# Optimization experiments

Measured on AMD Instinct MI355X. Metric: run time of the kernel, lower is better.

## Reference

```python
import jax, jax.numpy as jnp
import numpy as np


def setup_inputs() -> dict:
    key = jax.random.key(0)
    k1, k2, k3 = jax.random.split(key, 3)
    B, N, D = 4, 4096, 1024
    x = jax.random.normal(k1, (B, N, D), dtype=jnp.float32)
    # torch nn.Linear default init ~ U(-1/sqrt(D), 1/sqrt(D)); scale normals similarly
    scale = 1.0 / np.sqrt(D)
    Wq = jax.random.normal(k2, (D, D), dtype=jnp.float32) * scale
    Wk = jax.random.normal(k3, (D, D), dtype=jnp.float32) * scale
    return {"x": x, "Wq": Wq, "Wk": Wk}


def reference(x, Wq, Wk):
    # torch Linear: y = x @ W.T (weight shape [out, in])
    D = x.shape[-1]
    q = jnp.einsum('bnd,ed->bne', x, Wq)  # [B,N,D]
    k = jnp.einsum('bnd,ed->bne', x, Wk)  # [B,N,D]
    scores = jnp.einsum('bqd,bkd->bqk', q, k) / jnp.sqrt(jnp.float32(D))
    attn = jax.nn.softmax(scores, axis=-1)  # [B,N,N]
    return jnp.einsum('bqk,bkd->bqd', attn, x)
```

## Files before the change

### kernel.cpp

```cpp
#include <hip/hip_runtime.h>
#include <stdint.h>
#include <math.h>

typedef __attribute__((ext_vector_type(8))) short short8;
typedef __attribute__((ext_vector_type(4))) float fx4;
typedef unsigned int u32;

#define MFMA16(a, b, c) __builtin_amdgcn_mfma_f32_16x16x32_bf16(a, b, c, 0, 0, 0)
#define SCL 0.04508422002777948f

#define CFENCE asm volatile("" ::: "memory")

__device__ __forceinline__ unsigned short f2bfu(float f) {
  unsigned u = __builtin_bit_cast(unsigned, f);
  u += 0x7fffu + ((u >> 16) & 1u);
  return (unsigned short)(u >> 16);
}

__device__ __forceinline__ float fast_exp2(float x) {
  float r;
  asm("v_exp_f32 %0, %1" : "=v"(r) : "v"(x));
  return r;
}

__device__ __forceinline__ void gl_lds16(const void* g, void* l) {
  __builtin_amdgcn_global_load_lds(
      (const __attribute__((address_space(1))) u32*)g,
      (__attribute__((address_space(3))) u32*)l, 16, 0, 0);
}

__device__ __forceinline__ void barx() {
  CFENCE;
  __builtin_amdgcn_s_barrier();
  CFENCE;
}

__global__ __launch_bounds__(256) void prep_kernel(const float* __restrict__ x,
                                                   unsigned short* __restrict__ xT,
                                                   unsigned short* __restrict__ xbf) {
  __shared__ float tile[64 * 65];
  const int b = blockIdx.z, n0 = blockIdx.x * 64, d0 = blockIdx.y * 64;
  const int tid = threadIdx.x;
  const float* xb = x + ((size_t)b * 4096 + n0) * 1024 + d0;
#pragma unroll
  for (int i = 0; i < 4; i++) {
    int idx = tid + 256 * i;
    int r = idx >> 4, c4 = (idx & 15) * 4;
    const float4 v = *(const float4*)(xb + (size_t)r * 1024 + c4);
    float* tp = &tile[r * 65 + c4];
    tp[0] = v.x; tp[1] = v.y; tp[2] = v.z; tp[3] = v.w;
    uint2 pkt;
    pkt.x = (u32)f2bfu(v.x) | ((u32)f2bfu(v.y) << 16);
    pkt.y = (u32)f2bfu(v.z) | ((u32)f2bfu(v.w) << 16);
    *(uint2*)(xbf + ((size_t)b * 4096 + n0 + r) * 1024 + d0 + c4) = pkt;
  }
  __syncthreads();
  unsigned short* xo = xT + ((size_t)b * 1024 + d0) * 4096 + n0;
#pragma unroll
  for (int i = 0; i < 4; i++) {
    int idx = tid + 256 * i;
    int dr = idx >> 4, n4 = (idx & 15) * 4;
    unsigned short h0 = f2bfu(tile[(n4 + 0) * 65 + dr]);
    unsigned short h1 = f2bfu(tile[(n4 + 1) * 65 + dr]);
    unsigned short h2 = f2bfu(tile[(n4 + 2) * 65 + dr]);
    unsigned short h3 = f2bfu(tile[(n4 + 3) * 65 + dr]);
    uint2 pkt;
    pkt.x = (u32)h0 | ((u32)h1 << 16);
    pkt.y = (u32)h2 | ((u32)h3 << 16);
    *(uint2*)(xo + (size_t)dr * 4096 + n4) = pkt;
  }
}

__global__ __launch_bounds__(256) void wconv_kernel(const float* __restrict__ Wq,
                                                    const float* __restrict__ Wk,
                                                    unsigned short* __restrict__ Wqb,
                                                    unsigned short* __restrict__ Wkb) {
  int gid = blockIdx.x * 256 + threadIdx.x;
  const float* s = (gid < 262144) ? Wq : Wk;
  unsigned short* d = (gid < 262144) ? Wqb : Wkb;
  int off = (gid & 262143) * 4;
  const float4 v = *(const float4*)(s + off);
  uint2 pkt;
  pkt.x = (u32)f2bfu(v.x) | ((u32)f2bfu(v.y) << 16);
  pkt.y = (u32)f2bfu(v.z) | ((u32)f2bfu(v.w) << 16);
  *(uint2*)(d + off) = pkt;
}

__device__ __forceinline__ void core256(const unsigned short* __restrict__ Ab,
                                        const unsigned short* __restrict__ Bb,
                                        char* lp, fx4 (&acc)[8][4]) {
  constexpr int NT = 16;
  const int tid = threadIdx.x;
  const int wave = tid >> 6, lane = tid & 63;
  const int wm = wave >> 2, wn = wave & 3;
  const int quad = lane >> 4, l16 = lane & 15;

  const int sr0 = tid >> 3, so0 = (tid & 7) ^ (sr0 & 7);
  const int ga0 = sr0 * 1024 + so0 * 8;
  const int ga1 = ga0 + 64 * 1024;
  const int ld0 = tid * 16;

  const int cst0 = (quad ^ (l16 & 7)) * 16;
  const int cst1 = ((4 + quad) ^ (l16 & 7)) * 16;
  const int arb = wm * 16384 + l16 * 128;
  const int brb = 32768 + (wn >> 1) * 16384 + (wn & 1) * 8192 + l16 * 128;

#pragma unroll
  for (int i = 0; i < 8; i++)
#pragma unroll
    for (int j = 0; j < 4; j++) acc[i][j] = (fx4)0.f;

#define C_STG(OPb, halfb, rowadd, bufb, kte)                                        \
  do {                                                                              \
    gl_lds16(OPb + (size_t)(rowadd) * 1024 + (kte) + ga0, lp + (bufb) + (halfb) + ld0); \
    gl_lds16(OPb + (size_t)(rowadd) * 1024 + (kte) + ga1,                           \
             lp + (bufb) + (halfb) + ld0 + 8192);                                   \
  } while (0)

  C_STG(Bb, 32768, 0, 0, 0);
  C_STG(Ab, 0, 0, 0, 0);
  C_STG(Ab, 16384, 128, 0, 0);
  C_STG(Bb, 49152, 128, 0, 0);
  C_STG(Bb, 32768, 0, 65536, 64);
  C_STG(Ab, 0, 0, 65536, 64);
  asm volatile("s_waitcnt vmcnt(4)" ::: "memory");
  barx();

  short8 af[8], bf0[4], bf1[4];
  for (int t = 0; t < NT; ++t) {
    const int cbo = (t & 1) * 65536, nbo = cbo ^ 65536;
    const int kt1 = ((t + 1) & (NT - 1)) * 64;
    const int kt2 = ((t + 2) & (NT - 1)) * 64;
#pragma unroll
    for (int mt = 0; mt < 4; mt++) {
      af[2 * mt] = *(const short8*)(lp + cbo + arb + mt * 2048 + cst0);
      af[2 * mt + 1] = *(const short8*)(lp + cbo + arb + mt * 2048 + cst1);
    }
#pragma unroll
    for (int nt = 0; nt < 2; nt++) {
      bf0[2 * nt] = *(const short8*)(lp + cbo + brb + nt * 2048 + cst0);
      bf0[2 * nt + 1] = *(const short8*)(lp + cbo + brb + nt * 2048 + cst1);
    }
    C_STG(Ab, 16384, 128, nbo, kt1);
    barx();
    __builtin_amdgcn_s_setprio(1);
#pragma unroll
    for (int mt = 0; mt < 4; mt++)
#pragma unroll
      for (int nt = 0; nt < 2; nt++) {
        acc[mt][nt] = MFMA16(af[2 * mt], bf0[2 * nt], acc[mt][nt]);
        acc[mt][nt] = MFMA16(af[2 * mt + 1], bf0[2 * nt + 1], acc[mt][nt]);
      }
    __builtin_amdgcn_s_setprio(0);
    barx();
#pragma unroll
    for (int nt = 0; nt < 2; nt++) {
      bf1[2 * nt] = *(const short8*)(lp + cbo + brb + (nt + 2) * 2048 + cst0);
      bf1[2 * nt + 1] = *(const short8*)(lp + cbo + brb + (nt + 2) * 2048 + cst1);
    }
    C_STG(Bb, 49152, 128, nbo, kt1);
    barx();
    __builtin_amdgcn_s_setprio(1);
#pragma unroll
    for (int mt = 0; mt < 4; mt++)
#pragma unroll
      for (int nt = 0; nt < 2; nt++) {
        acc[mt][nt + 2] = MFMA16(af[2 * mt], bf1[2 * nt], acc[mt][nt + 2]);
        acc[mt][nt + 2] = MFMA16(af[2 * mt + 1], bf1[2 * nt + 1], acc[mt][nt + 2]);
      }
    __builtin_amdgcn_s_setprio(0);
    barx();
#pragma unroll
    for (int mt = 0; mt < 4; mt++) {
      af[2 * mt] = *(const short8*)(lp + cbo + arb + (mt + 4) * 2048 + cst0);
      af[2 * mt + 1] = *(const short8*)(lp + cbo + arb + (mt + 4) * 2048 + cst1);
    }
    C_STG(Bb, 32768, 0, cbo, kt2);
    barx();
    __builtin_amdgcn_s_setprio(1);
#pragma unroll
    for (int mt = 0; mt < 4; mt++)
#pragma unroll
      for (int nt = 0; nt < 2; nt++) {
        acc[mt + 4][nt + 2] = MFMA16(af[2 * mt], bf1[2 * nt], acc[mt + 4][nt + 2]);
        acc[mt + 4][nt + 2] = MFMA16(af[2 * mt + 1], bf1[2 * nt + 1], acc[mt + 4][nt + 2]);
      }
    __builtin_amdgcn_s_setprio(0);
    barx();
    C_STG(Ab, 0, 0, cbo, kt2);
    asm volatile("s_waitcnt vmcnt(4)" ::: "memory");
    barx();
    __builtin_amdgcn_s_setprio(1);
#pragma unroll
    for (int mt = 0; mt < 4; mt++)
#pragma unroll
      for (int nt = 0; nt < 2; nt++) {
        acc[mt + 4][nt] = MFMA16(af[2 * mt], bf0[2 * nt], acc[mt + 4][nt]);
        acc[mt + 4][nt] = MFMA16(af[2 * mt + 1], bf0[2 * nt + 1], acc[mt + 4][nt]);
      }
    __builtin_amdgcn_s_setprio(0);
    barx();
  }
#undef C_STG
}

template <int ONES, int NT, int LDA, int LDB>
__device__ __forceinline__ void core128(const unsigned short* __restrict__ Ab,
                                        const unsigned short* __restrict__ Bb,
                                        short* lds, fx4 (&acc)[4][4], fx4 (&accl)[4]) {
  constexpr int BUFB = 49152;
  const int tid = threadIdx.x;
  const int wave = tid >> 6, lane = tid & 63;
  const int wm = wave >> 1, wn = wave & 1;
  const int quad = lane >> 4, l16 = lane & 15;
  char* lp = (char*)lds;

  const int sr0 = tid >> 3, so0 = (tid & 7) ^ (sr0 & 7);
  const int ga0 = sr0 * LDA + so0 * 8;
  const int ga1 = ga0 + 64 * LDA;
  const int gb0 = sr0 * LDB + so0 * 8;
  const int ld0 = tid * 16;

  const int cst0 = (quad ^ (l16 & 7)) * 16;
  const int cst1 = ((4 + quad) ^ (l16 & 7)) * 16;
  const int arb = (wm >> 1) * 16384 + (wm & 1) * 8192 + l16 * 128;
  const int brb = 32768 + wn * 8192 + l16 * 128;

  short8 ones;
#pragma unroll
  for (int i = 0; i < 8; i++) ones[i] = (short)0x3F80;
#pragma unroll
  for (int i = 0; i < 4; i++) {
    accl[i] = (fx4)0.f;
#pragma unroll
    for (int j = 0; j < 4; j++) acc[i][j] = (fx4)0.f;
  }

#define PV_STGA(halfb, rowadd, bufb, kte)                                          \
  do {                                                                             \
    gl_lds16(Ab + (size_t)(rowadd) * LDA + (kte) + ga0, lp + (bufb) + (halfb) + ld0); \
    gl_lds16(Ab + (size_t)(rowadd) * LDA + (kte) + ga1,                            \
             lp + (bufb) + (halfb) + ld0 + 8192);                                  \
  } while (0)
#define PV_STGB(halfb, rowadd, bufb, kte) \
  gl_lds16(Bb + (size_t)(rowadd) * LDB + (kte) + gb0, lp + (bufb) + 32768 + (halfb) + ld0)

  PV_STGB(0, 0, 0, 0);
  PV_STGA(0, 0, 0, 0);
  PV_STGA(16384, 128, 0, 0);
  PV_STGB(8192, 64, 0, 0);
  PV_STGB(0, 0, BUFB, 64);
  PV_STGA(0, 0, BUFB, 64);
  asm volatile("s_waitcnt vmcnt(3)" ::: "memory");
  barx();

  short8 af[4], bf0[4], bf1[4];
  for (int t = 0; t < NT; ++t) {
    const int cbo = (t & 1) * BUFB, nbo = cbo ^ BUFB;
    const int kt1 = ((t + 1) & (NT - 1)) * 64;
    const int kt2 = ((t + 2) & (NT - 1)) * 64;
#pragma unroll
    for (int mt = 0; mt < 2; mt++) {
      af[2 * mt] = *(const short8*)(lp + cbo + arb + mt * 2048 + cst0);
      af[2 * mt + 1] = *(const short8*)(lp + cbo + arb + mt * 2048 + cst1);
    }
#pragma unroll
    for (int nt = 0; nt < 2; nt++) {
      bf0[2 * nt] = *(const short8*)(lp + cbo + brb + nt * 2048 + cst0);
      bf0[2 * nt + 1] = *(const short8*)(lp + cbo + brb + nt * 2048 + cst1);
    }
    PV_STGA(16384, 128, nbo, kt1);
    barx();
    __builtin_amdgcn_s_setprio(1);
#pragma unroll
    for (int mt = 0; mt < 2; mt++) {
#pragma unroll
      for (int nt = 0; nt < 2; nt++) {
        acc[mt][nt] = MFMA16(af[2 * mt], bf0[2 * nt], acc[mt][nt]);
        acc[mt][nt] = MFMA16(af[2 * mt + 1], bf0[2 * nt + 1], acc[mt][nt]);
      }
      if (ONES) {
        accl[mt] = MFMA16(af[2 * mt], ones, accl[mt]);
        accl[mt] = MFMA16(af[2 * mt + 1], ones, accl[mt]);
      }
    }
    __builtin_amdgcn_s_setprio(0);
    barx();
#pragma unroll
    for (int nt = 0; nt < 2; nt++) {
      bf1[2 * nt] = *(const short8*)(lp + cbo + brb + (nt + 2) * 2048 + cst0);
      bf1[2 * nt + 1] = *(const short8*)(lp + cbo + brb + (nt + 2) * 2048 + cst1);
    }
    PV_STGB(8192, 64, nbo, kt1);
    barx();
    __builtin_amdgcn_s_setprio(1);
#pragma unroll
    for (int mt = 0; mt < 2; mt++)
#pragma unroll
      for (int nt = 0; nt < 2; nt++) {
        acc[mt][nt + 2] = MFMA16(af[2 * mt], bf1[2 * nt], acc[mt][nt + 2]);
        acc[mt][nt + 2] = MFMA16(af[2 * mt + 1], bf1[2 * nt + 1], acc[mt][nt + 2]);
      }
    __builtin_amdgcn_s_setprio(0);
    barx();
#pragma unroll
    for (int mt = 0; mt < 2; mt++) {
      af[2 * mt] = *(const short8*)(lp + cbo + arb + (mt + 2) * 2048 + cst0);
      af[2 * mt + 1] = *(const short8*)(lp + cbo + arb + (mt + 2) * 2048 + cst1);
    }
    PV_STGB(0, 0, cbo, kt2);
    barx();
    __builtin_amdgcn_s_setprio(1);
#pragma unroll
    for (int mt = 0; mt < 2; mt++) {
#pragma unroll
      for (int nt = 0; nt < 2; nt++) {
        acc[mt + 2][nt + 2] = MFMA16(af[2 * mt], bf1[2 * nt], acc[mt + 2][nt + 2]);
        acc[mt + 2][nt + 2] = MFMA16(af[2 * mt + 1], bf1[2 * nt + 1], acc[mt + 2][nt + 2]);
      }
      if (ONES) {
        accl[mt + 2] = MFMA16(af[2 * mt], ones, accl[mt + 2]);
        accl[mt + 2] = MFMA16(af[2 * mt + 1], ones, accl[mt + 2]);
      }
    }
    __builtin_amdgcn_s_setprio(0);
    barx();
    PV_STGA(0, 0, cbo, kt2);
    asm volatile("s_waitcnt vmcnt(3)" ::: "memory");
    barx();
    __builtin_amdgcn_s_setprio(1);
#pragma unroll
    for (int mt = 0; mt < 2; mt++)
#pragma unroll
      for (int nt = 0; nt < 2; nt++) {
        acc[mt + 2][nt] = MFMA16(af[2 * mt], bf0[2 * nt], acc[mt + 2][nt]);
        acc[mt + 2][nt] = MFMA16(af[2 * mt + 1], bf0[2 * nt + 1], acc[mt + 2][nt]);
      }
    __builtin_amdgcn_s_setprio(0);
    barx();
  }
#undef PV_STGA
#undef PV_STGB
}

__global__ __launch_bounds__(512) void proj_kernel(
    const unsigned short* __restrict__ xbf, const unsigned short* __restrict__ Wqb,
    const unsigned short* __restrict__ Wkb, unsigned short* __restrict__ Qo,
    unsigned short* __restrict__ Ko) {
  __shared__ __attribute__((aligned(16))) short lds[65536];
  const unsigned short* Wb = blockIdx.z ? Wkb : Wqb;
  unsigned short* O = blockIdx.z ? Ko : Qo;
  const int m0 = blockIdx.x * 256, e0 = blockIdx.y * 256;
  fx4 acc[8][4];
  core256(xbf + (size_t)m0 * 1024, Wb + (size_t)e0 * 1024, (char*)lds, acc);
  const int wave = threadIdx.x >> 6, lane = threadIdx.x & 63;
  const int wm = wave >> 2, wn = wave & 3;
  const int quad = lane >> 4, l16 = lane & 15;
#pragma unroll
  for (int mt = 0; mt < 8; mt++) {
    const int row = m0 + wm * 128 + mt * 16 + quad * 4;
#pragma unroll
    for (int nt = 0; nt < 4; nt++) {
      const int col = e0 + wn * 64 + nt * 16 + l16;
      unsigned short* op = O + (size_t)row * 1024 + col;
#pragma unroll
      for (int i = 0; i < 4; i++) op[(size_t)i * 1024] = f2bfu(acc[mt][nt][i]);
    }
  }
}

__global__ __launch_bounds__(512) void qk_kernel(
    const unsigned short* __restrict__ Qb, const unsigned short* __restrict__ Kb,
    unsigned short* __restrict__ Pp, int bbase) {
  __shared__ __attribute__((aligned(16))) short lds[65536];
  const int bz = blockIdx.z, b = bbase + bz;
  unsigned short* Pb = Pp + (size_t)bz * 4096 * 4096;
  const int m0 = blockIdx.x * 256, n0 = blockIdx.y * 256;
  fx4 acc[8][4];
  core256(Qb + (size_t)b * 4096 * 1024 + (size_t)m0 * 1024,
          Kb + (size_t)b * 4096 * 1024 + (size_t)n0 * 1024, (char*)lds, acc);
  const int wave = threadIdx.x >> 6, lane = threadIdx.x & 63;
  const int wm = wave >> 2, wn = wave & 3;
  const int quad = lane >> 4, l16 = lane & 15;
#pragma unroll
  for (int mt = 0; mt < 8; mt++) {
    const int row = m0 + wm * 128 + mt * 16 + quad * 4;
#pragma unroll
    for (int nt = 0; nt < 4; nt++) {
      const int col = n0 + wn * 64 + nt * 16 + l16;
      unsigned short* pp = Pb + (size_t)row * 4096 + col;
#pragma unroll
      for (int i = 0; i < 4; i++)
        pp[(size_t)i * 4096] = f2bfu(fast_exp2(acc[mt][nt][i] * SCL));
    }
  }
}

__global__ __launch_bounds__(512) void pv_kernel(
    const unsigned short* __restrict__ P, const unsigned short* __restrict__ xT,
    unsigned short* __restrict__ Ost, int bbase) {
  __shared__ __attribute__((aligned(16))) short lds[49152];
  const int bz = blockIdx.z, b = bbase + bz;
  const int m0 = blockIdx.x * 256, e0 = blockIdx.y * 128;
  const unsigned short* Ab = P + (size_t)bz * 4096 * 4096 + (size_t)m0 * 4096;
  const unsigned short* Bb = xT + (size_t)b * 1024 * 4096 + (size_t)e0 * 4096;
  fx4 acc[4][4], accl[4];
  core128<1, 64, 4096, 4096>(Ab, Bb, lds, acc, accl);
  unsigned short* O = Ost + (size_t)b * 4096 * 1024;
  const int wave = threadIdx.x >> 6, lane = threadIdx.x & 63;
  const int wm = wave >> 1, wn = wave & 1;
  const int quad = lane >> 4, l16 = lane & 15;
#pragma unroll
  for (int mt = 0; mt < 4; mt++) {
    const int row = m0 + wm * 64 + mt * 16 + quad * 4;
    const fx4 li = accl[mt];
    fx4 r;
#pragma unroll
    for (int i = 0; i < 4; i++) r[i] = __builtin_amdgcn_rcpf(li[i]);
#pragma unroll
    for (int nt = 0; nt < 4; nt++) {
      const int col = e0 + wn * 64 + nt * 16 + l16;
      unsigned short* op = O + (size_t)row * 1024 + col;
#pragma unroll
      for (int i = 0; i < 4; i++) op[(size_t)i * 1024] = f2bfu(acc[mt][nt][i] * r[i]);
    }
  }
}

__global__ __launch_bounds__(256) void fin_kernel(const uint4* __restrict__ Ost,
                                                  float4* __restrict__ out) {
  size_t t = (size_t)blockIdx.x * 256 + threadIdx.x;
  const uint4 v = Ost[t];
  float4 o0, o1;
  o0.x = __builtin_bit_cast(float, v.x << 16);
  o0.y = __builtin_bit_cast(float, v.x & 0xffff0000u);
  o0.z = __builtin_bit_cast(float, v.y << 16);
  o0.w = __builtin_bit_cast(float, v.y & 0xffff0000u);
  o1.x = __builtin_bit_cast(float, v.z << 16);
  o1.y = __builtin_bit_cast(float, v.z & 0xffff0000u);
  o1.z = __builtin_bit_cast(float, v.w << 16);
  o1.w = __builtin_bit_cast(float, v.w & 0xffff0000u);
  out[t * 2] = o0;
  out[t * 2 + 1] = o1;
}

extern "C" void kernel_launch(void* const* d_in, const int* in_sizes, int n_in,
                              void* d_out, int out_size, void* d_ws, size_t ws_size,
                              hipStream_t stream) {
  const float* x = (const float*)d_in[0];
  const float* Wq = (const float*)d_in[1];
  const float* Wk = (const float*)d_in[2];
  char* ws = (char*)d_ws;
  unsigned short* xT = (unsigned short*)ws;
  unsigned short* Qb = (unsigned short*)(ws + (size_t)33554432);
  unsigned short* Kb = (unsigned short*)(ws + (size_t)67108864);
  unsigned short* Ost = Qb;
  unsigned short* xbf = (unsigned short*)d_out;
  unsigned short* Wqb = (unsigned short*)((char*)d_out + (size_t)33554432);
  unsigned short* Wkb = (unsigned short*)((char*)d_out + (size_t)35651584);
  unsigned short* Pp = (unsigned short*)d_out;

  hipLaunchKernelGGL(prep_kernel, dim3(64, 16, 4), dim3(256), 0, stream, x, xT, xbf);
  hipLaunchKernelGGL(wconv_kernel, dim3(2048), dim3(256), 0, stream, Wq, Wk, Wqb, Wkb);
  hipLaunchKernelGGL(proj_kernel, dim3(64, 4, 2), dim3(512), 0, stream, xbf, Wqb, Wkb, Qb, Kb);
  hipLaunchKernelGGL(qk_kernel, dim3(16, 16, 2), dim3(512), 0, stream, Qb, Kb, Pp, 0);
  hipLaunchKernelGGL(pv_kernel, dim3(16, 8, 2), dim3(512), 0, stream, Pp, xT, Ost, 0);
  hipLaunchKernelGGL(qk_kernel, dim3(16, 16, 2), dim3(512), 0, stream, Qb, Kb, Pp, 2);
  hipLaunchKernelGGL(pv_kernel, dim3(16, 8, 2), dim3(512), 0, stream, Pp, xT, Ost, 2);
  hipLaunchKernelGGL(fin_kernel, dim3(8192), dim3(256), 0, stream,
                     (const uint4*)Ost, (float4*)d_out);
}
```

Baseline: 486.7 us.

## Shrink PV kernel tile to 256x64 with new core64 pipeline, doubling grid

Replaces the 256x128 PV GEMM tile core with a 256x64 variant. Each of the 8 waves now owns 32 rows by 64 columns, the LDS footprint shrinks, and launch bounds ask for more blocks per CU. The grid doubles to 16x16x2, which gives more parallelism and occupancy for the PV GEMM. In exchange the P matrix is read twice as often from memory, and the ones-MFMA row-sum work per output column doubles.

```diff
diff --git a/kernel.cpp b/kernel.cpp
--- a/kernel.cpp
+++ b/kernel.cpp
@@ -204,16 +204,14 @@
 #undef C_STG
 }
 
-template <int ONES, int NT, int LDA, int LDB>
-__device__ __forceinline__ void core128(const unsigned short* __restrict__ Ab,
-                                        const unsigned short* __restrict__ Bb,
-                                        short* lds, fx4 (&acc)[4][4], fx4 (&accl)[4]) {
-  constexpr int BUFB = 49152;
+template <int NT, int LDA, int LDB>
+__device__ __forceinline__ void core64(const unsigned short* __restrict__ Ab,
+                                       const unsigned short* __restrict__ Bb,
+                                       char* lp, fx4 (&acc)[2][4], fx4 (&accl)[2]) {
+  constexpr int BUFB = 40960;
   const int tid = threadIdx.x;
   const int wave = tid >> 6, lane = tid & 63;
-  const int wm = wave >> 1, wn = wave & 1;
   const int quad = lane >> 4, l16 = lane & 15;
-  char* lp = (char*)lds;
 
   const int sr0 = tid >> 3, so0 = (tid & 7) ^ (sr0 & 7);
   const int ga0 = sr0 * LDA + so0 * 8;
@@ -223,67 +221,55 @@
 
   const int cst0 = (quad ^ (l16 & 7)) * 16;
   const int cst1 = ((4 + quad) ^ (l16 & 7)) * 16;
-  const int arb = (wm >> 1) * 16384 + (wm & 1) * 8192 + l16 * 128;
-  const int brb = 32768 + wn * 8192 + l16 * 128;
+  const int arb = (wave >> 2) * 16384 + ((wave & 3) * 32 + l16) * 128;
+  const int brb = 32768 + l16 * 128;
 
   short8 ones;
 #pragma unroll
   for (int i = 0; i < 8; i++) ones[i] = (short)0x3F80;
 #pragma unroll
-  for (int i = 0; i < 4; i++) {
+  for (int i = 0; i < 2; i++) {
     accl[i] = (fx4)0.f;
 #pragma unroll
     for (int j = 0; j < 4; j++) acc[i][j] = (fx4)0.f;
   }
 
-#define PV_STGA(halfb, rowadd, bufb, kte)                                          \
+#define C64_STGA(halfb, rowadd, bufb, kte)                                         \
   do {                                                                             \
     gl_lds16(Ab + (size_t)(rowadd) * LDA + (kte) + ga0, lp + (bufb) + (halfb) + ld0); \
     gl_lds16(Ab + (size_t)(rowadd) * LDA + (kte) + ga1,                            \
              lp + (bufb) + (halfb) + ld0 + 8192);                                  \
   } while (0)
-#define PV_STGB(halfb, rowadd, bufb, kte) \
-  gl_lds16(Bb + (size_t)(rowadd) * LDB + (kte) + gb0, lp + (bufb) + 32768 + (halfb) + ld0)
-
-  PV_STGB(0, 0, 0, 0);
-  PV_STGA(0, 0, 0, 0);
-  PV_STGA(16384, 128, 0, 0);
-  PV_STGB(8192, 64, 0, 0);
-  PV_STGB(0, 0, BUFB, 64);
-  PV_STGA(0, 0, BUFB, 64);
-  asm volatile("s_waitcnt vmcnt(3)" ::: "memory");
+#define C64_STGB(bufb, kte) gl_lds16(Bb + (size_t)(kte) + gb0, lp + (bufb) + 32768 + ld0)
+
+  C64_STGA(0, 0, 0, 0);
+  C64_STGA(16384, 128, 0, 0);
+  C64_STGB(0, 0);
+  C64_STGA(0, 0, BUFB, 64);
+  asm volatile("s_waitcnt vmcnt(2)" ::: "memory");
   barx();
 
-  short8 af[4], bf0[4], bf1[4];
+  short8 af0[2], af1[2], bf0[4], bf1[4];
   for (int t = 0; t < NT; ++t) {
     const int cbo = (t & 1) * BUFB, nbo = cbo ^ BUFB;
     const int kt1 = ((t + 1) & (NT - 1)) * 64;
     const int kt2 = ((t + 2) & (NT - 1)) * 64;
-#pragma unroll
-    for (int mt = 0; mt < 2; mt++) {
-      af[2 * mt] = *(const short8*)(lp + cbo + arb + mt * 2048 + cst0);
-      af[2 * mt + 1] = *(const short8*)(lp + cbo + arb + mt * 2048 + cst1);
-    }
+    af0[0] = *(const short8*)(lp + cbo + arb + cst0);
+    af0[1] = *(const short8*)(lp + cbo + arb + cst1);
 #pragma unroll
     for (int nt = 0; nt < 2; nt++) {
       bf0[2 * nt] = *(const short8*)(lp + cbo + brb + nt * 2048 + cst0);
       bf0[2 * nt + 1] = *(const short8*)(lp + cbo + brb + nt * 2048 + cst1);
     }
-    PV_STGA(16384, 128, nbo, kt1);
-    barx();
-    __builtin_amdgcn_s_setprio(1);
-#pragma unroll
-    for (int mt = 0; mt < 2; mt++) {
-#pragma unroll
-      for (int nt = 0; nt < 2; nt++) {
-        acc[mt][nt] = MFMA16(af[2 * mt], bf0[2 * nt], acc[mt][nt]);
-        acc[mt][nt] = MFMA16(af[2 * mt + 1], bf0[2 * nt + 1], acc[mt][nt]);
-      }
-      if (ONES) {
-        accl[mt] = MFMA16(af[2 * mt], ones, accl[mt]);
-        accl[mt] = MFMA16(af[2 * mt + 1], ones, accl[mt]);
-      }
-    }
+    C64_STGA(16384, 128, nbo, kt1);
+    barx();
+    __builtin_amdgcn_s_setprio(1);
+    acc[0][0] = MFMA16(af0[0], bf0[0], acc[0][0]);
+    acc[0][0] = MFMA16(af0[1], bf0[1], acc[0][0]);
+    acc[0][1] = MFMA16(af0[0], bf0[2], acc[0][1]);
+    acc[0][1] = MFMA16(af0[1], bf0[3], acc[0][1]);
+    accl[0] = MFMA16(af0[0], ones, accl[0]);
+    accl[0] = MFMA16(af0[1], ones, accl[0]);
     __builtin_amdgcn_s_setprio(0);
     barx();
 #pragma unroll
@@ -291,56 +277,40 @@
       bf1[2 * nt] = *(const short8*)(lp + cbo + brb + (nt + 2) * 2048 + cst0);
       bf1[2 * nt + 1] = *(const short8*)(lp + cbo + brb + (nt + 2) * 2048 + cst1);
     }
-    PV_STGB(8192, 64, nbo, kt1);
-    barx();
-    __builtin_amdgcn_s_setprio(1);
-#pragma unroll
-    for (int mt = 0; mt < 2; mt++)
-#pragma unroll
-      for (int nt = 0; nt < 2; nt++) {
-        acc[mt][nt + 2] = MFMA16(af[2 * mt], bf1[2 * nt], acc[mt][nt + 2]);
-        acc[mt][nt + 2] = MFMA16(af[2 * mt + 1], bf1[2 * nt + 1], acc[mt][nt + 2]);
-      }
-    __builtin_amdgcn_s_setprio(0);
-    barx();
-#pragma unroll
-    for (int mt = 0; mt < 2; mt++) {
-      af[2 * mt] = *(const short8*)(lp + cbo + arb + (mt + 2) * 2048 + cst0);
-      af[2 * mt + 1] = *(const short8*)(lp + cbo + arb + (mt + 2) * 2048 + cst1);
-    }
-    PV_STGB(0, 0, cbo, kt2);
-    barx();
-    __builtin_amdgcn_s_setprio(1);
-#pragma unroll
-    for (int mt = 0; mt < 2; mt++) {
-#pragma unroll
-      for (int nt = 0; nt < 2; nt++) {
-        acc[mt + 2][nt + 2] = MFMA16(af[2 * mt], bf1[2 * nt], acc[mt + 2][nt + 2]);
-        acc[mt + 2][nt + 2] = MFMA16(af[2 * mt + 1], bf1[2 * nt + 1], acc[mt + 2][nt + 2]);
-      }
-      if (ONES) {
-        accl[mt + 2] = MFMA16(af[2 * mt], ones, accl[mt + 2]);
-        accl[mt + 2] = MFMA16(af[2 * mt + 1], ones, accl[mt + 2]);
-      }
-    }
-    __builtin_amdgcn_s_setprio(0);
-    barx();
-    PV_STGA(0, 0, cbo, kt2);
-    asm volatile("s_waitcnt vmcnt(3)" ::: "memory");
-    barx();
-    __builtin_amdgcn_s_setprio(1);
-#pragma unroll
-    for (int mt = 0; mt < 2; mt++)
-#pragma unroll
-      for (int nt = 0; nt < 2; nt++) {
-        acc[mt + 2][nt] = MFMA16(af[2 * mt], bf0[2 * nt], acc[mt + 2][nt]);
-        acc[mt + 2][nt] = MFMA16(af[2 * mt + 1], bf0[2 * nt + 1], acc[mt + 2][nt]);
-      }
-    __builtin_amdgcn_s_setprio(0);
-    barx();
-  }
-#undef PV_STGA
-#undef PV_STGB
+    C64_STGB(nbo, kt1);
+    barx();
+    __builtin_amdgcn_s_setprio(1);
+    acc[0][2] = MFMA16(af0[0], bf1[0], acc[0][2]);
+    acc[0][2] = MFMA16(af0[1], bf1[1], acc[0][2]);
+    acc[0][3] = MFMA16(af0[0], bf1[2], acc[0][3]);
+    acc[0][3] = MFMA16(af0[1], bf1[3], acc[0][3]);
+    __builtin_amdgcn_s_setprio(0);
+    barx();
+    af1[0] = *(const short8*)(lp + cbo + arb + 2048 + cst0);
+    af1[1] = *(const short8*)(lp + cbo + arb + 2048 + cst1);
+    barx();
+    __builtin_amdgcn_s_setprio(1);
+    acc[1][2] = MFMA16(af1[0], bf1[0], acc[1][2]);
+    acc[1][2] = MFMA16(af1[1], bf1[1], acc[1][2]);
+    acc[1][3] = MFMA16(af1[0], bf1[2], acc[1][3]);
+    acc[1][3] = MFMA16(af1[1], bf1[3], acc[1][3]);
+    accl[1] = MFMA16(af1[0], ones, accl[1]);
+    accl[1] = MFMA16(af1[1], ones, accl[1]);
+    __builtin_amdgcn_s_setprio(0);
+    barx();
+    C64_STGA(0, 0, cbo, kt2);
+    asm volatile("s_waitcnt vmcnt(2)" ::: "memory");
+    barx();
+    __builtin_amdgcn_s_setprio(1);
+    acc[1][0] = MFMA16(af1[0], bf0[0], acc[1][0]);
+    acc[1][0] = MFMA16(af1[1], bf0[1], acc[1][0]);
+    acc[1][1] = MFMA16(af1[0], bf0[2], acc[1][1]);
+    acc[1][1] = MFMA16(af1[1], bf0[3], acc[1][1]);
+    __builtin_amdgcn_s_setprio(0);
+    barx();
+  }
+#undef C64_STGA
+#undef C64_STGB
 }
 
 __global__ __launch_bounds__(512) void proj_kernel(
@@ -396,30 +366,29 @@
   }
 }
 
-__global__ __launch_bounds__(512) void pv_kernel(
+__global__ __launch_bounds__(512, 4) void pv_kernel(
     const unsigned short* __restrict__ P, const unsigned short* __restrict__ xT,
     unsigned short* __restrict__ Ost, int bbase) {
-  __shared__ __attribute__((aligned(16))) short lds[49152];
+  __shared__ __attribute__((aligned(16))) short lds[40960];
   const int bz = blockIdx.z, b = bbase + bz;
-  const int m0 = blockIdx.x * 256, e0 = blockIdx.y * 128;
+  const int m0 = blockIdx.x * 256, e0 = blockIdx.y * 64;
   const unsigned short* Ab = P + (size_t)bz * 4096 * 4096 + (size_t)m0 * 4096;
   const unsigned short* Bb = xT + (size_t)b * 1024 * 4096 + (size_t)e0 * 4096;
-  fx4 acc[4][4], accl[4];
-  core128<1, 64, 4096, 4096>(Ab, Bb, lds, acc, accl);
+  fx4 acc[2][4], accl[2];
+  core64<64, 4096, 4096>(Ab, Bb, (char*)lds, acc, accl);
   unsigned short* O = Ost + (size_t)b * 4096 * 1024;
   const int wave = threadIdx.x >> 6, lane = threadIdx.x & 63;
-  const int wm = wave >> 1, wn = wave & 1;
   const int quad = lane >> 4, l16 = lane & 15;
 #pragma unroll
-  for (int mt = 0; mt < 4; mt++) {
-    const int row = m0 + wm * 64 + mt * 16 + quad * 4;
+  for (int mt = 0; mt < 2; mt++) {
+    const int row = m0 + wave * 32 + mt * 16 + quad * 4;
     const fx4 li = accl[mt];
     fx4 r;
 #pragma unroll
     for (int i = 0; i < 4; i++) r[i] = __builtin_amdgcn_rcpf(li[i]);
 #pragma unroll
     for (int nt = 0; nt < 4; nt++) {
-      const int col = e0 + wn * 64 + nt * 16 + l16;
+      const int col = e0 + nt * 16 + l16;
       unsigned short* op = O + (size_t)row * 1024 + col;
 #pragma unroll
       for (int i = 0; i < 4; i++) op[(size_t)i * 1024] = f2bfu(acc[mt][nt][i] * r[i]);
@@ -464,9 +433,9 @@
   hipLaunchKernelGGL(wconv_kernel, dim3(2048), dim3(256), 0, stream, Wq, Wk, Wqb, Wkb);
   hipLaunchKernelGGL(proj_kernel, dim3(64, 4, 2), dim3(512), 0, stream, xbf, Wqb, Wkb, Qb, Kb);
   hipLaunchKernelGGL(qk_kernel, dim3(16, 16, 2), dim3(512), 0, stream, Qb, Kb, Pp, 0);
-  hipLaunchKernelGGL(pv_kernel, dim3(16, 8, 2), dim3(512), 0, stream, Pp, xT, Ost, 0);
+  hipLaunchKernelGGL(pv_kernel, dim3(16, 16, 2), dim3(512), 0, stream, Pp, xT, Ost, 0);
   hipLaunchKernelGGL(qk_kernel, dim3(16, 16, 2), dim3(512), 0, stream, Qb, Kb, Pp, 2);
-  hipLaunchKernelGGL(pv_kernel, dim3(16, 8, 2), dim3(512), 0, stream, Pp, xT, Ost, 2);
+  hipLaunchKernelGGL(pv_kernel, dim3(16, 16, 2), dim3(512), 0, stream, Pp, xT, Ost, 2);
   hipLaunchKernelGGL(fin_kernel, dim3(8192), dim3(256), 0, stream,
                      (const uint4*)Ost, (float4*)d_out);
 }
```

Measured after the change: 500.3 us. +2.8%, slower.
